# Performance work log

Measured on AMD Instinct MI355X. Metric: run time of the kernel, lower is better.

The kernel has to match this reference:

```python
import jax, jax.numpy as jnp
import numpy as np

H = 12          # n_heads
TYPE = 0        # center node type (query path)
EDGES = (0, 4, 5)  # useful_edge for type==0
NEG = -1e10
LN_EPS = 1e-5


def _type_emb(x, W, b, t):
    # Linear(E -> 2E), view [N,2,E], scatter-mask select type t (uniform type -> index)
    h = x @ W.T + b
    N = x.shape[0]
    E = W.shape[0] // 2
    return h.reshape(N, 2, E)[:, t, :]


def _layernorm(x, g, b):
    mu = jnp.mean(x, axis=-1, keepdims=True)
    var = jnp.mean((x - mu) ** 2, axis=-1, keepdims=True)
    return g * (x - mu) / jnp.sqrt(var + LN_EPS) + b


def setup_inputs() -> dict:
    B, L, E, R = 64, 64, 768, 8
    dk = E // H
    key = jax.random.key(0)
    ks = jax.random.split(key, 16)
    s = 0.02
    inp = {
        'center_ids': jax.random.randint(ks[0], (B, L), 0, 5000),
        'centers': jax.random.normal(ks[1], (B * L, E), jnp.float32),
        'all_embs': jax.random.normal(ks[2], (2 * B * L, E), jnp.float32),
        'pre_mask': (jax.random.uniform(ks[3], (B, L, L)) < 0.3).astype(jnp.float32),
        'back_mask': (jax.random.uniform(ks[4], (B, L, L)) < 0.3).astype(jnp.float32),
        'click_mask': (jax.random.uniform(ks[5], (B, L, L)) < 0.3).astype(jnp.float32),
        'blank': jnp.zeros((B, L, L), jnp.float32),
        'Wq': jax.random.normal(ks[6], (2 * E, E), jnp.float32) * s,
        'bq': jnp.zeros((2 * E,), jnp.float32),
        'Wk': jax.random.normal(ks[7], (2 * E, E), jnp.float32) * s,
        'bk': jnp.zeros((2 * E,), jnp.float32),
        'Wv': jax.random.normal(ks[8], (2 * E, E), jnp.float32) * s,
        'bv': jnp.zeros((2 * E,), jnp.float32),
        'Wa': jax.random.normal(ks[9], (2 * E, E), jnp.float32) * s,
        'ba': jnp.zeros((2 * E,), jnp.float32),
        'relation_pri': jnp.ones((R, H), jnp.float32),
        'relation_att': jax.random.normal(ks[10], (R, H, dk, dk), jnp.float32) / np.sqrt(dk),
        'relation_msg': jax.random.normal(ks[11], (R, H, dk, dk), jnp.float32) / np.sqrt(dk),
        'skip': jnp.ones((3,), jnp.float32),
        'ln_gamma': jnp.ones((E,), jnp.float32),
        'ln_beta': jnp.zeros((E,), jnp.float32),
    }
    return inp


def reference(center_ids, centers, all_embs, pre_mask, back_mask, click_mask, blank,
              Wq, bq, Wk, bk, Wv, bv, Wa, ba,
              relation_pri, relation_att, relation_msg, skip, ln_gamma, ln_beta):
    B, L = center_ids.shape
    E = centers.shape[-1]
    dk = E // H
    BL = B * L
    sqrt_dk = np.sqrt(dk).astype(np.float32)

    # type-masked QKV projections (q: all type 0; k,v: first BL type 0, second BL type 1)
    q = _type_emb(centers, Wq, bq, TYPE)                       # [BL, E]
    hk = (all_embs @ Wk.T + bk).reshape(2 * BL, 2, E)
    k = jnp.concatenate([hk[:BL, 0], hk[BL:, 1]], axis=0)      # [2BL, E]
    hv = (all_embs @ Wv.T + bv).reshape(2 * BL, 2, E)
    v = jnp.concatenate([hv[:BL, 0], hv[BL:, 1]], axis=0)      # [2BL, E]

    q4 = q.reshape(B, L, H, dk).transpose(2, 0, 1, 3)                          # [H,B,L,dk]
    k4 = k.reshape(2, B, L, H, dk).transpose(3, 1, 0, 2, 4).reshape(H, B, 2 * L, dk)
    v4 = v.reshape(2, B, L, H, dk).transpose(3, 1, 0, 2, 4).reshape(H, B, 2 * L, dk)

    eidx = jnp.array(EDGES)
    ra = relation_att[eidx]   # [3,H,dk,dk]
    rm = relation_msg[eidx]   # [3,H,dk,dk]
    pri = relation_pri[eidx]  # [3,H]

    kproj = jnp.einsum('hbtd,ehdf->ehbtf', k4, ra)                                  # [3,H,B,2L,dk]
    att = jnp.einsum('hbld,ehbtd->ehblt', q4, kproj) * pri[:, :, None, None, None] / sqrt_dk
    msg = jnp.einsum('hbtd,ehdf->ehbtf', v4, rm)                                    # [3,H,B,2L,dk]

    # flatten (kv_pos, edge) in the torch cat/view order: index = t*3 + e
    A = att.transpose(1, 2, 3, 4, 0).reshape(H, B, L, 2 * L * 3)
    msgf = msg.transpose(1, 2, 3, 0, 4).reshape(H, B, 2 * L * 3, dk)

    # per-edge masks for type==0: edge0 -> [blank|click], edge1 -> [back|blank], edge2 -> [pre|blank]
    m0 = jnp.concatenate([blank, click_mask], axis=-1)
    m1 = jnp.concatenate([back_mask, blank], axis=-1)
    m2 = jnp.concatenate([pre_mask, blank], axis=-1)
    mask = jnp.stack([m0, m1, m2], axis=-1).reshape(B, L, 2 * L * 3) > 0            # [B,L,TE]

    # share masks among identical center ids (equality is transitive => one matmul = closure)
    same = center_ids[:, :, None] == center_ids[:, None, :]                         # [B,L,L]
    repeat = jnp.triu(same, 1).sum(1) > 0                                           # [B,L]
    add = jnp.einsum('bil,blj->bij', same.astype(jnp.float32), mask.astype(jnp.float32)) > 0
    mask = (mask | add) & (~repeat[:, :, None])

    scores = jnp.where(mask[None], A, NEG)
    p = jax.nn.softmax(scores, axis=-1) * mask[None].astype(A.dtype)
    neigh = jnp.einsum('hblt,hbtd->hbld', p, msgf).transpose(1, 2, 0, 3).reshape(BL, E)
    neigh = jax.nn.gelu(neigh, approximate=False)

    retype = _type_emb(neigh, Wa, ba, TYPE)
    alpha = jax.nn.sigmoid(skip[TYPE])
    res = retype * alpha + centers * (1.0 - alpha)
    out = _layernorm(res, ln_gamma, ln_beta)
    return out.reshape(B, L, E)
```

## Files before the change

### kernel.cpp

```cpp
#include <hip/hip_runtime.h>
#include <cmath>

#define NEGV -1e10f

typedef __bf16 bf16_t;
typedef bf16_t bf16x8 __attribute__((ext_vector_type(8)));
typedef bf16_t bf16x4 __attribute__((ext_vector_type(4)));
typedef float f32x4 __attribute__((ext_vector_type(4)));

typedef const __attribute__((address_space(1))) void* gas1p;
typedef __attribute__((address_space(3))) void* las3p;

__global__ __launch_bounds__(256)
void f2b6_kernel(const float* __restrict__ s0, bf16_t* __restrict__ d0,
                 const float* __restrict__ s1, bf16_t* __restrict__ d1,
                 const float* __restrict__ s2, bf16_t* __restrict__ d2,
                 const float* __restrict__ s3, bf16_t* __restrict__ d3,
                 const float* __restrict__ s4, bf16_t* __restrict__ d4,
                 const float* __restrict__ s5, bf16_t* __restrict__ d5) {
  const int N0=786432, N1=1572864, N2=147456, N3=294912, N4=294912, N5=147456;
  const int T = N0+N1+N2+N3+N4+N5;
  int i = blockIdx.x * 256 + threadIdx.x;
  const int stride = gridDim.x * 256;
  for (; i < T; i += stride) {
    const float* s; bf16_t* d; int j = i;
    if (j < N0) { s = s0; d = d0; }
    else { j -= N0; if (j < N1) { s = s1; d = d1; }
    else { j -= N1; if (j < N2) { s = s2; d = d2; }
    else { j -= N2; if (j < N3) { s = s3; d = d3; }
    else { j -= N3; if (j < N4) { s = s4; d = d4; }
    else { j -= N4; s = s5; d = d5; } } } } }
    float4 v = *(const float4*)(s + (size_t)j * 4);
    bf16x4 o = { (bf16_t)v.x, (bf16_t)v.y, (bf16_t)v.z, (bf16_t)v.w };
    *(bf16x4*)(d + (size_t)j * 4) = o;
  }
}

__global__ __launch_bounds__(256)
void fold_rm(const float* __restrict__ rmsg, bf16_t* __restrict__ rmT) {
  const int eh = blockIdx.x;
  const int e = eh / 12, h = eh - e*12;
  const int re = (e==0) ? 0 : (e==1 ? 4 : 5);
  const int tid = threadIdx.x;
  for (int i = 0; i < 16; ++i) {
    int idx = i*256 + tid;
    int d = idx >> 6, f = idx & 63;
    rmT[((size_t)(e*12 + h)*64 + d)*64 + f] =
        (bf16_t)rmsg[((size_t)(re*12 + h)*64 + f)*64 + d];
  }
}

template<int NCOLS, int WSTRIDE, int BSTRIDE, int MHALF>
__global__ __launch_bounds__(256)
void proj_mfmaB(const bf16_t* __restrict__ X, const bf16_t* __restrict__ W,
                const float* __restrict__ bias, bf16_t* __restrict__ Y) {
  __shared__ bf16_t As[128 * 32];
  __shared__ bf16_t Bs[128 * 32];
  const int bn = blockIdx.x, bm = blockIdx.y;
  const int s = (MHALF && bm >= MHALF) ? 1 : 0;
  const int row0 = bm * 128, col0 = bn * 128;
  const int tid = threadIdx.x, wave = tid >> 6, lane = tid & 63;
  const int wr = wave >> 1, wc = wave & 1;
  f32x4 acc[4][4] = {};
  const int arow = wr * 64 + (lane & 15);
  const int bcol = wc * 64 + (lane & 15);
  const int koff = (lane >> 4) * 8;
  const bf16_t* Wb = W + (size_t)s * WSTRIDE;
  for (int k0 = 0; k0 < 768; k0 += 32) {
    __syncthreads();
    #pragma unroll
    for (int i = 0; i < 2; ++i) {
      int c = i * 256 + tid; int r = c >> 2; int c8 = (c & 3) * 8;
      __builtin_amdgcn_global_load_lds((gas1p)(X  + (size_t)(row0 + r) * 768 + k0 + c8),
                                       (las3p)(As + c * 8), 16, 0, 0);
      __builtin_amdgcn_global_load_lds((gas1p)(Wb + (size_t)(col0 + r) * 768 + k0 + c8),
                                       (las3p)(Bs + c * 8), 16, 0, 0);
    }
    __syncthreads();
    bf16x8 af[4], bfr[4];
    #pragma unroll
    for (int m = 0; m < 4; ++m) af[m]  = *(const bf16x8*)(As + (arow + m * 16) * 32 + koff);
    #pragma unroll
    for (int n = 0; n < 4; ++n) bfr[n] = *(const bf16x8*)(Bs + (bcol + n * 16) * 32 + koff);
    #pragma unroll
    for (int m = 0; m < 4; ++m)
      #pragma unroll
      for (int n = 0; n < 4; ++n)
        acc[m][n] = __builtin_amdgcn_mfma_f32_16x16x32_bf16(af[m], bfr[n], acc[m][n], 0, 0, 0);
  }
  const int ocol0 = col0 + wc * 64 + (lane & 15);
  const int orow0 = row0 + wr * 64 + (lane >> 4) * 4;
  #pragma unroll
  for (int n = 0; n < 4; ++n) {
    const int col = ocol0 + n * 16;
    const float bvl = bias[s * BSTRIDE + col];
    #pragma unroll
    for (int m = 0; m < 4; ++m)
      #pragma unroll
      for (int r = 0; r < 4; ++r)
        Y[(size_t)(orow0 + m * 16 + r) * NCOLS + col] = (bf16_t)(acc[m][n][r] + bvl);
  }
}

__global__ __launch_bounds__(256)
void proj_mfmaF(const bf16_t* __restrict__ X, const bf16_t* __restrict__ W,
                const float* __restrict__ bias, float* __restrict__ Y) {
  __shared__ bf16_t As[128 * 32];
  __shared__ bf16_t Bs[128 * 32];
  const int bn = blockIdx.x, bm = blockIdx.y;
  const int row0 = bm * 128, col0 = bn * 128;
  const int tid = threadIdx.x, wave = tid >> 6, lane = tid & 63;
  const int wr = wave >> 1, wc = wave & 1;
  f32x4 acc[4][4] = {};
  const int arow = wr * 64 + (lane & 15);
  const int bcol = wc * 64 + (lane & 15);
  const int koff = (lane >> 4) * 8;
  for (int k0 = 0; k0 < 768; k0 += 32) {
    __syncthreads();
    #pragma unroll
    for (int i = 0; i < 2; ++i) {
      int c = i * 256 + tid; int r = c >> 2; int c8 = (c & 3) * 8;
      __builtin_amdgcn_global_load_lds((gas1p)(X + (size_t)(row0 + r) * 768 + k0 + c8),
                                       (las3p)(As + c * 8), 16, 0, 0);
      __builtin_amdgcn_global_load_lds((gas1p)(W + (size_t)(col0 + r) * 768 + k0 + c8),
                                       (las3p)(Bs + c * 8), 16, 0, 0);
    }
    __syncthreads();
    bf16x8 af[4], bfr[4];
    #pragma unroll
    for (int m = 0; m < 4; ++m) af[m]  = *(const bf16x8*)(As + (arow + m * 16) * 32 + koff);
    #pragma unroll
    for (int n = 0; n < 4; ++n) bfr[n] = *(const bf16x8*)(Bs + (bcol + n * 16) * 32 + koff);
    #pragma unroll
    for (int m = 0; m < 4; ++m)
      #pragma unroll
      for (int n = 0; n < 4; ++n)
        acc[m][n] = __builtin_amdgcn_mfma_f32_16x16x32_bf16(af[m], bfr[n], acc[m][n], 0, 0, 0);
  }
  const int ocol0 = col0 + wc * 64 + (lane & 15);
  const int orow0 = row0 + wr * 64 + (lane >> 4) * 4;
  #pragma unroll
  for (int n = 0; n < 4; ++n) {
    const int col = ocol0 + n * 16;
    const float bvl = bias[col];
    #pragma unroll
    for (int m = 0; m < 4; ++m)
      #pragma unroll
      for (int r = 0; r < 4; ++r)
        Y[(size_t)(orow0 + m * 16 + r) * 768 + col] = acc[m][n][r] + bvl;
  }
}

template<int WSTRIDE, int BSTRIDE>
__global__ __launch_bounds__(256)
void projT(const bf16_t* __restrict__ X, const bf16_t* __restrict__ W,
           const float* __restrict__ bias, bf16_t* __restrict__ YT) {
  __shared__ bf16_t As[128 * 32];
  __shared__ bf16_t Bs[128 * 32];
  __shared__ char tl[128 * 256];
  const int bn = blockIdx.x, bm = blockIdx.y;
  const int s = (bm >= 32) ? 1 : 0;
  const int row0 = bm * 128, col0 = bn * 128;
  const int tid = threadIdx.x, wave = tid >> 6, lane = tid & 63;
  const int wr = wave >> 1, wc = wave & 1;
  f32x4 acc[4][4] = {};
  const int arow = wr * 64 + (lane & 15);
  const int bcol = wc * 64 + (lane & 15);
  const int koff = (lane >> 4) * 8;
  const bf16_t* Wb = W + (size_t)s * WSTRIDE;
  for (int k0 = 0; k0 < 768; k0 += 32) {
    __syncthreads();
    #pragma unroll
    for (int i = 0; i < 2; ++i) {
      int c = i * 256 + tid; int r = c >> 2; int c8 = (c & 3) * 8;
      __builtin_amdgcn_global_load_lds((gas1p)(X  + (size_t)(row0 + r) * 768 + k0 + c8),
                                       (las3p)(As + c * 8), 16, 0, 0);
      __builtin_amdgcn_global_load_lds((gas1p)(Wb + (size_t)(col0 + r) * 768 + k0 + c8),
                                       (las3p)(Bs + c * 8), 16, 0, 0);
    }
    __syncthreads();
    bf16x8 af[4], bfr[4];
    #pragma unroll
    for (int m = 0; m < 4; ++m) af[m]  = *(const bf16x8*)(As + (arow + m * 16) * 32 + koff);
    #pragma unroll
    for (int n = 0; n < 4; ++n) bfr[n] = *(const bf16x8*)(Bs + (bcol + n * 16) * 32 + koff);
    #pragma unroll
    for (int m = 0; m < 4; ++m)
      #pragma unroll
      for (int n = 0; n < 4; ++n)
        acc[m][n] = __builtin_amdgcn_mfma_f32_16x16x32_bf16(af[m], bfr[n], acc[m][n], 0, 0, 0);
  }
  __syncthreads();
  #pragma unroll
  for (int n = 0; n < 4; ++n) {
    const int cl = wc * 64 + n * 16 + (lane & 15);
    const float bvl = bias[s * BSTRIDE + col0 + cl];
    #pragma unroll
    for (int m = 0; m < 4; ++m)
      #pragma unroll
      for (int r = 0; r < 4; ++r) {
        const int rl = wr * 64 + m * 16 + (lane >> 4) * 4 + r;
        *(bf16_t*)(tl + ((cl * 256 + rl * 2) ^ ((cl & 7) << 4))) = (bf16_t)(acc[m][n][r] + bvl);
      }
  }
  __syncthreads();
  for (int i = 0; i < 8; ++i) {
    int idx = i * 256 + tid; int c = idx >> 4; int t0 = (idx & 15) * 8;
    bf16x8 v = *(const bf16x8*)(tl + ((c * 256 + t0 * 2) ^ ((c & 7) << 4)));
    *(bf16x8*)(YT + (size_t)(col0 + c) * 8192 + row0 + t0) = v;
  }
}

__global__ __launch_bounds__(256)
void qtrans_kernel(const bf16_t* __restrict__ qraw, const float* __restrict__ ratt,
                   const float* __restrict__ pri, bf16_t* __restrict__ qeb) {
  const int eh = blockIdx.x;
  const int e = eh / 12, h = eh - e*12;
  const int re = (e==0) ? 0 : (e==1 ? 4 : 5);
  const int row0 = blockIdx.y * 128;
  const float scale = pri[re*12 + h] * 0.125f;
  __shared__ char qls[128 * 128];
  __shared__ char rals[64 * 128];
  const int tid = threadIdx.x, wave = tid >> 6, lane = tid & 63;
  const int colb = lane & 15;
  for (int i = 0; i < 4; ++i) {
    int idx = i*256 + tid;
    int l = idx >> 3, f0 = (idx & 7) * 8;
    bf16x8 v = *(const bf16x8*)(qraw + (size_t)(row0 + l)*768 + h*64 + f0);
    *(bf16x8*)(qls + ((l*128 + f0*2) ^ ((l & 7) << 4))) = v;
  }
  for (int i = 0; i < 4; ++i) {
    int idx = i*256 + tid;
    int d = idx >> 4, f0 = (idx & 15) * 4;
    float4 v = *(const float4*)(ratt + ((size_t)(re*12 + h)*64 + d)*64 + f0);
    bf16x4 o = { (bf16_t)v.x, (bf16_t)v.y, (bf16_t)v.z, (bf16_t)v.w };
    *(bf16x4*)(rals + ((d*128 + f0*2) ^ ((d & 7) << 4))) = o;
  }
  __syncthreads();
  f32x4 acc[2][4] = {};
  #pragma unroll
  for (int ks = 0; ks < 2; ++ks) {
    const int kb2 = (ks*32 + (lane >> 4)*8) * 2;
    bf16x8 bfr[4];
    #pragma unroll
    for (int n = 0; n < 4; ++n) {
      int d = n*16 + colb;
      bfr[n] = *(const bf16x8*)(rals + ((d*128 + kb2) ^ ((d & 7) << 4)));
    }
    #pragma unroll
    for (int m = 0; m < 2; ++m) {
      int l = wave*32 + m*16 + colb;
      bf16x8 a = *(const bf16x8*)(qls + ((l*128 + kb2) ^ ((l & 7) << 4)));
      #pragma unroll
      for (int n = 0; n < 4; ++n)
        acc[m][n] = __builtin_amdgcn_mfma_f32_16x16x32_bf16(a, bfr[n], acc[m][n], 0, 0, 0);
    }
  }
  #pragma unroll
  for (int m = 0; m < 2; ++m)
    #pragma unroll
    for (int n = 0; n < 4; ++n)
      #pragma unroll
      for (int r = 0; r < 4; ++r) {
        int l = wave*32 + m*16 + (lane >> 4)*4 + r;
        int d = n*16 + colb;
        qeb[(size_t)(row0 + l)*2304 + (e*12 + h)*64 + d] = (bf16_t)(scale * acc[m][n][r]);
      }
}

__global__ __launch_bounds__(256)
void mask_kernel(const int* __restrict__ ids, const float* __restrict__ pre,
                 const float* __restrict__ back, const float* __restrict__ click,
                 unsigned long long* __restrict__ msk64) {
  const int b = blockIdx.x, tid = threadIdx.x;
  __shared__ float pm[64][68], bmm[64][68], cm[64][68];
  __shared__ unsigned long long sbits[64];
  __shared__ unsigned long long colbits[384];
  __shared__ int sid[64];
  __shared__ unsigned char srep[64];
  for (int r = 0; r < 4; ++r) {
    int idx = r*256 + tid; int row = idx >> 4; int c4 = (idx & 15) * 4;
    *(float4*)&pm[row][c4]  = *(const float4*)(pre   + (size_t)b*4096 + row*64 + c4);
    *(float4*)&bmm[row][c4] = *(const float4*)(back  + (size_t)b*4096 + row*64 + c4);
    *(float4*)&cm[row][c4]  = *(const float4*)(click + (size_t)b*4096 + row*64 + c4);
  }
  if (tid < 64) sid[tid] = ids[b*64 + tid];
  __syncthreads();
  if (tid < 64) {
    int myid = sid[tid];
    unsigned long long bits = 0ull; int rep = 0;
    for (int l = 0; l < 64; ++l) {
      bool eq = (sid[l] == myid);
      bits |= ((unsigned long long)eq) << l;
      rep |= (eq && (l < tid)) ? 1 : 0;
    }
    sbits[tid] = bits; srep[tid] = (unsigned char)rep;
  }
  for (int j = tid; j < 384; j += 256) {
    int e = j >> 7, t = j & 127;
    unsigned long long cb = 0ull;
    if (e == 0) {
      if (t >= 64) { int tt = t - 64; for (int l = 0; l < 64; ++l) cb |= ((unsigned long long)(cm[l][tt] > 0.0f)) << l; }
    } else if (e == 1) {
      if (t < 64) { for (int l = 0; l < 64; ++l) cb |= ((unsigned long long)(bmm[l][t] > 0.0f)) << l; }
    } else {
      if (t < 64) { for (int l = 0; l < 64; ++l) cb |= ((unsigned long long)(pm[l][t] > 0.0f)) << l; }
    }
    colbits[j] = cb;
  }
  __syncthreads();
  for (int idx = tid; idx < 384; idx += 256) {
    int l = idx / 6, w = idx - l*6;
    unsigned long long r = 0ull;
    if (!srep[l]) {
      unsigned long long sb = sbits[l];
      const int base = w*64;
      for (int jj = 0; jj < 64; ++jj)
        r |= (unsigned long long)((sb & colbits[base + jj]) != 0ull) << jj;
    }
    msk64[((size_t)(b*64) + l)*6 + w] = r;
  }
}

__global__ __launch_bounds__(256, 2)
void attn_fused(const bf16_t* __restrict__ qeb, const bf16_t* __restrict__ kb,
                const bf16_t* __restrict__ vT, const bf16_t* __restrict__ rmT,
                const unsigned long long* __restrict__ msk64,
                bf16_t* __restrict__ neigh) {
  const int h = blockIdx.x, b = blockIdx.y;
  __shared__ char kls[128 * 128];
  __shared__ char vls[64 * 256];
  __shared__ char rmls[3][64 * 128];
  __shared__ char pls[64 * 256];
  __shared__ char us[64 * 128];
  const int tid = threadIdx.x, wave = tid >> 6, lane = tid & 63;
  const int band = wave * 16;
  const int colb = lane & 15;
  for (int i = 0; i < 4; ++i) {
    int idx = i*256 + tid;
    int t = idx >> 3, c8 = (idx & 7) * 8;
    int srow = (t >> 6)*4096 + b*64 + (t & 63);
    bf16x8 v = *(const bf16x8*)(kb + (size_t)srow*768 + h*64 + c8);
    *(bf16x8*)(kls + ((t*128 + c8*2) ^ ((t & 7) << 4))) = v;
  }
  for (int i = 0; i < 4; ++i) {
    int idx = i*256 + tid;
    int f = idx >> 4, t0 = (idx & 15) * 8;
    bf16x8 v = *(const bf16x8*)(vT + (size_t)(h*64 + f)*8192 + (t0 >> 6)*4096 + b*64 + (t0 & 63));
    *(bf16x8*)(vls + ((f*256 + t0*2) ^ ((f & 7) << 4))) = v;
  }
  for (int i = 0; i < 6; ++i) {
    int idx = i*256 + tid;
    int e = idx >> 9, rem = idx & 511, d = rem >> 3, f0 = (rem & 7) * 8;
    bf16x8 v = *(const bf16x8*)(rmT + (size_t)((e*12 + h)*64 + d)*64 + f0);
    *(bf16x8*)(rmls[e] + ((d*128 + f0*2) ^ ((d & 7) << 4))) = v;
  }
  bf16x8 af[3][2];
  #pragma unroll
  for (int e = 0; e < 3; ++e)
    #pragma unroll
    for (int ks = 0; ks < 2; ++ks)
      af[e][ks] = *(const bf16x8*)(qeb + (size_t)(b*64 + band + colb)*2304
                                   + (e*12 + h)*64 + ks*32 + (lane >> 4)*8);
  __syncthreads();
  f32x4 acc[3][8] = {};
  #pragma unroll
  for (int ks = 0; ks < 2; ++ks) {
    bf16x8 bfr[8];
    #pragma unroll
    for (int n = 0; n < 8; ++n) {
      int t = n*16 + colb;
      bfr[n] = *(const bf16x8*)(kls + ((t*128 + (ks*32 + (lane >> 4)*8)*2) ^ ((t & 7) << 4)));
    }
    #pragma unroll
    for (int e = 0; e < 3; ++e)
      #pragma unroll
      for (int n = 0; n < 8; ++n)
        acc[e][n] = __builtin_amdgcn_mfma_f32_16x16x32_bf16(af[e][ks], bfr[n], acc[e][n], 0, 0, 0);
  }
  float mx[4], inv[4];
  #pragma unroll
  for (int r = 0; r < 4; ++r) {
    const int l = band + (lane >> 4)*4 + r;
    const unsigned long long* mr = msk64 + (size_t)(b*64 + l)*6;
    #pragma unroll
    for (int e = 0; e < 3; ++e) {
      unsigned long long w0 = mr[e*2], w1 = mr[e*2 + 1];
      #pragma unroll
      for (int n = 0; n < 8; ++n) {
        unsigned long long w = (n < 4) ? w0 : w1;
        int bitpos = (n*16 + colb) & 63;
        if (!((w >> bitpos) & 1ull)) acc[e][n][r] = NEGV;
      }
    }
  }
  #pragma unroll
  for (int r = 0; r < 4; ++r) {
    float m = NEGV;
    #pragma unroll
    for (int e = 0; e < 3; ++e)
      #pragma unroll
      for (int n = 0; n < 8; ++n) m = fmaxf(m, acc[e][n][r]);
    #pragma unroll
    for (int off = 1; off < 16; off <<= 1) m = fmaxf(m, __shfl_xor(m, off, 64));
    mx[r] = m;
  }
  #pragma unroll
  for (int r = 0; r < 4; ++r) {
    float s = 0.0f;
    #pragma unroll
    for (int e = 0; e < 3; ++e)
      #pragma unroll
      for (int n = 0; n < 8; ++n) {
        float v = __expf(acc[e][n][r] - mx[r]);
        acc[e][n][r] = v; s += v;
      }
    #pragma unroll
    for (int off = 1; off < 16; off <<= 1) s += __shfl_xor(s, off, 64);
    inv[r] = (mx[r] < -5e9f) ? 0.0f : 1.0f / s;
  }
  f32x4 accN[4] = {};
  #pragma unroll
  for (int e = 0; e < 3; ++e) {
    #pragma unroll
    for (int n = 0; n < 8; ++n)
      #pragma unroll
      for (int r = 0; r < 4; ++r) {
        int l = band + (lane >> 4)*4 + r;
        int t = n*16 + colb;
        *(bf16_t*)(pls + ((l*256 + t*2) ^ ((l & 7) << 4))) = (bf16_t)(acc[e][n][r] * inv[r]);
      }
    __syncthreads();
    f32x4 accU[4] = {};
    #pragma unroll
    for (int ks = 0; ks < 4; ++ks) {
      const int kb2 = (ks*32 + (lane >> 4)*8) * 2;
      const int la = band + colb;
      bf16x8 a = *(const bf16x8*)(pls + ((la*256 + kb2) ^ ((la & 7) << 4)));
      #pragma unroll
      for (int n = 0; n < 4; ++n) {
        int f = n*16 + colb;
        bf16x8 bv = *(const bf16x8*)(vls + ((f*256 + kb2) ^ ((f & 7) << 4)));
        accU[n] = __builtin_amdgcn_mfma_f32_16x16x32_bf16(a, bv, accU[n], 0, 0, 0);
      }
    }
    #pragma unroll
    for (int n = 0; n < 4; ++n)
      #pragma unroll
      for (int r = 0; r < 4; ++r) {
        int l = band + (lane >> 4)*4 + r;
        int f = n*16 + colb;
        *(bf16_t*)(us + ((l*128 + f*2) ^ ((l & 7) << 4))) = (bf16_t)accU[n][r];
      }
    __syncthreads();
    #pragma unroll
    for (int ks = 0; ks < 2; ++ks) {
      const int kb2 = (ks*32 + (lane >> 4)*8) * 2;
      const int la = band + colb;
      bf16x8 a2 = *(const bf16x8*)(us + ((la*128 + kb2) ^ ((la & 7) << 4)));
      #pragma unroll
      for (int n = 0; n < 4; ++n) {
        int d = n*16 + colb;
        bf16x8 brm = *(const bf16x8*)(rmls[e] + ((d*128 + kb2) ^ ((d & 7) << 4)));
        accN[n] = __builtin_amdgcn_mfma_f32_16x16x32_bf16(a2, brm, accN[n], 0, 0, 0);
      }
    }
  }
  #pragma unroll
  for (int n = 0; n < 4; ++n)
    #pragma unroll
    for (int r = 0; r < 4; ++r) {
      int l = band + (lane >> 4)*4 + r;
      int d = n*16 + colb;
      float x = accN[n][r];
      float g = 0.5f * x * (1.0f + erff(x * 0.70710678118654752f));
      neigh[(size_t)(b*64 + l)*768 + h*64 + d] = (bf16_t)g;
    }
}

__global__ __launch_bounds__(256)
void ln_kernel(const float* __restrict__ rt, const float* __restrict__ centers,
               const float* __restrict__ skip, const float* __restrict__ gamma,
               const float* __restrict__ beta, float* __restrict__ out) {
  const int row  = blockIdx.x*4 + (threadIdx.x >> 6);
  const int lane = threadIdx.x & 63;
  const float alpha = 1.0f / (1.0f + expf(-skip[0]));
  const float* rp = rt + (size_t)row*768;
  const float* cp = centers + (size_t)row*768;
  float r[12];
  float sum = 0.0f;
  #pragma unroll
  for (int c = 0; c < 12; ++c) {
    int j = lane + 64*c;
    float x = alpha*rp[j] + (1.0f - alpha)*cp[j];
    r[c] = x; sum += x;
  }
  #pragma unroll
  for (int off = 1; off < 64; off <<= 1) sum += __shfl_xor(sum, off, 64);
  float mean = sum * (1.0f/768.0f);
  float vsum = 0.0f;
  #pragma unroll
  for (int c = 0; c < 12; ++c) { float d = r[c] - mean; vsum += d*d; }
  #pragma unroll
  for (int off = 1; off < 64; off <<= 1) vsum += __shfl_xor(vsum, off, 64);
  float inv = 1.0f / sqrtf(vsum * (1.0f/768.0f) + 1e-5f);
  #pragma unroll
  for (int c = 0; c < 12; ++c) {
    int j = lane + 64*c;
    out[(size_t)row*768 + j] = gamma[j]*(r[c] - mean)*inv + beta[j];
  }
}

extern "C" void kernel_launch(void* const* d_in, const int* in_sizes, int n_in,
                              void* d_out, int out_size, void* d_ws, size_t ws_size,
                              hipStream_t stream) {
  const int*   ids     = (const int*)  d_in[0];
  const float* centers = (const float*)d_in[1];
  const float* allemb  = (const float*)d_in[2];
  const float* pre     = (const float*)d_in[3];
  const float* back    = (const float*)d_in[4];
  const float* click   = (const float*)d_in[5];
  const float* Wq = (const float*)d_in[7];
  const float* bq = (const float*)d_in[8];
  const float* Wk = (const float*)d_in[9];
  const float* bk = (const float*)d_in[10];
  const float* Wv = (const float*)d_in[11];
  const float* bv = (const float*)d_in[12];
  const float* Wa = (const float*)d_in[13];
  const float* ba = (const float*)d_in[14];
  const float* pri  = (const float*)d_in[15];
  const float* ratt = (const float*)d_in[16];
  const float* rmsg = (const float*)d_in[17];
  const float* skip = (const float*)d_in[18];
  const float* gam  = (const float*)d_in[19];
  const float* bet  = (const float*)d_in[20];
  float* out = (float*)d_out;

  char* wp = (char*)d_ws;
  bf16_t* cen_bf = (bf16_t*)wp;  wp += 6291456;
  bf16_t* all_bf = (bf16_t*)wp;  wp += 12582912;
  bf16_t* Wq_bf  = (bf16_t*)wp;  wp += 1179648;
  bf16_t* Wk_bf  = (bf16_t*)wp;  wp += 2359296;
  bf16_t* Wv_bf  = (bf16_t*)wp;  wp += 2359296;
  bf16_t* Wa_bf  = (bf16_t*)wp;  wp += 1179648;
  bf16_t* rmT    = (bf16_t*)wp;  wp += 294912;
  bf16_t* qraw   = (bf16_t*)wp;  wp += 6291456;
  bf16_t* qeb    = (bf16_t*)wp;  wp += 18874368;
  bf16_t* kb     = (bf16_t*)wp;  wp += 12582912;
  bf16_t* vTb    = (bf16_t*)wp;  wp += 12582912;
  unsigned long long* msk64 = (unsigned long long*)wp; wp += 196608;
  bf16_t* neighb = (bf16_t*)wp;  wp += 6291456;
  float*  rt     = (float*)wp;   wp += 12582912;

  f2b6_kernel<<<dim3(2048), 256, 0, stream>>>(centers, cen_bf, allemb, all_bf,
                                              Wq, Wq_bf, Wk, Wk_bf, Wv, Wv_bf, Wa, Wa_bf);
  fold_rm<<<dim3(36), 256, 0, stream>>>(rmsg, rmT);

  proj_mfmaB<768, 0, 0, 0>         <<<dim3(6, 32), 256, 0, stream>>>(cen_bf, Wq_bf, bq, qraw);
  qtrans_kernel                     <<<dim3(36, 32), 256, 0, stream>>>(qraw, ratt, pri, qeb);
  proj_mfmaB<768, 768*768, 768, 32><<<dim3(6, 64), 256, 0, stream>>>(all_bf, Wk_bf, bk, kb);
  projT<768*768, 768>              <<<dim3(6, 64), 256, 0, stream>>>(all_bf, Wv_bf, bv, vTb);

  mask_kernel<<<dim3(64), 256, 0, stream>>>(ids, pre, back, click, msk64);
  attn_fused<<<dim3(12, 64), 256, 0, stream>>>(qeb, kb, vTb, rmT, msk64, neighb);

  proj_mfmaF<<<dim3(6, 32), 256, 0, stream>>>(neighb, Wa_bf, ba, rt);
  ln_kernel<<<dim3(1024), 256, 0, stream>>>(rt, centers, skip, gam, bet, out);
}
```

Before: 271.0 us.

## Fuse prep kernels, merge K/V projections, and fold query relation transform into attention

Merges the mask build, relation-matrix folding and fp32-to-bf16 conversions into one prep launch. K and V projections now share a single kernel that loads each A tile once for both weight matrices. The per-relation query transform moves inside the attention kernel, which removes the qeb intermediate write and read and two launches. The costs are a larger LDS footprint in attention, which is reused through aliased regions, and extra register pressure from prefetching all operands into registers.

```diff
diff --git a/kernel.cpp b/kernel.cpp
--- a/kernel.cpp
+++ b/kernel.cpp
@@ -11,17 +11,91 @@
 typedef const __attribute__((address_space(1))) void* gas1p;
 typedef __attribute__((address_space(3))) void* las3p;
 
+#define MFMA __builtin_amdgcn_mfma_f32_16x16x32_bf16
+
 __global__ __launch_bounds__(256)
-void f2b6_kernel(const float* __restrict__ s0, bf16_t* __restrict__ d0,
+void prep_kernel(const int* __restrict__ ids, const float* __restrict__ pre,
+                 const float* __restrict__ back, const float* __restrict__ click,
+                 unsigned long long* __restrict__ msk64,
+                 const float* __restrict__ rmsg, const float* __restrict__ ratt,
+                 const float* __restrict__ pri, bf16_t* __restrict__ rmT, bf16_t* __restrict__ raB,
+                 const float* __restrict__ s0, bf16_t* __restrict__ d0,
                  const float* __restrict__ s1, bf16_t* __restrict__ d1,
                  const float* __restrict__ s2, bf16_t* __restrict__ d2,
                  const float* __restrict__ s3, bf16_t* __restrict__ d3,
                  const float* __restrict__ s4, bf16_t* __restrict__ d4,
                  const float* __restrict__ s5, bf16_t* __restrict__ d5) {
+  const int bid = blockIdx.x, tid = threadIdx.x;
+  __shared__ float pm[64][68], bmm[64][68], cm[64][68];
+  __shared__ unsigned long long sbits[64];
+  __shared__ unsigned long long colbits[384];
+  __shared__ int sid[64];
+  __shared__ unsigned char srep[64];
+  if (bid < 64) {
+    const int b = bid;
+    for (int r = 0; r < 4; ++r) {
+      int idx = r*256 + tid; int row = idx >> 4; int c4 = (idx & 15) * 4;
+      *(float4*)&pm[row][c4]  = *(const float4*)(pre   + (size_t)b*4096 + row*64 + c4);
+      *(float4*)&bmm[row][c4] = *(const float4*)(back  + (size_t)b*4096 + row*64 + c4);
+      *(float4*)&cm[row][c4]  = *(const float4*)(click + (size_t)b*4096 + row*64 + c4);
+    }
+    if (tid < 64) sid[tid] = ids[b*64 + tid];
+    __syncthreads();
+    if (tid < 64) {
+      int myid = sid[tid];
+      unsigned long long bits = 0ull; int rep = 0;
+      for (int l = 0; l < 64; ++l) {
+        bool eq = (sid[l] == myid);
+        bits |= ((unsigned long long)eq) << l;
+        rep |= (eq && (l < tid)) ? 1 : 0;
+      }
+      sbits[tid] = bits; srep[tid] = (unsigned char)rep;
+    }
+    for (int j = tid; j < 384; j += 256) {
+      int e = j >> 7, t = j & 127;
+      unsigned long long cb = 0ull;
+      if (e == 0) {
+        if (t >= 64) { int tt = t - 64; for (int l = 0; l < 64; ++l) cb |= ((unsigned long long)(cm[l][tt] > 0.0f)) << l; }
+      } else if (e == 1) {
+        if (t < 64) { for (int l = 0; l < 64; ++l) cb |= ((unsigned long long)(bmm[l][t] > 0.0f)) << l; }
+      } else {
+        if (t < 64) { for (int l = 0; l < 64; ++l) cb |= ((unsigned long long)(pm[l][t] > 0.0f)) << l; }
+      }
+      colbits[j] = cb;
+    }
+    __syncthreads();
+    for (int idx = tid; idx < 384; idx += 256) {
+      int l = idx / 6, w = idx - l*6;
+      unsigned long long r = 0ull;
+      if (!srep[l]) {
+        unsigned long long sb = sbits[l];
+        const int base = w*64;
+        for (int jj = 0; jj < 64; ++jj)
+          r |= (unsigned long long)((sb & colbits[base + jj]) != 0ull) << jj;
+      }
+      msk64[((size_t)(b*64) + l)*6 + w] = r;
+    }
+    return;
+  }
+  if (bid < 100) {
+    const int eh = bid - 64;
+    const int e = eh / 12, h = eh - e*12;
+    const int re = (e==0) ? 0 : (e==1 ? 4 : 5);
+    const float scale = pri[re*12 + h] * 0.125f;
+    for (int i = 0; i < 16; ++i) {
+      int idx = i*256 + tid;
+      int d = idx >> 6, f = idx & 63;
+      rmT[((size_t)(e*12 + h)*64 + d)*64 + f] =
+          (bf16_t)rmsg[((size_t)(re*12 + h)*64 + f)*64 + d];
+      raB[((size_t)(e*12 + h)*64 + d)*64 + f] =
+          (bf16_t)(ratt[((size_t)(re*12 + h)*64 + d)*64 + f] * scale);
+    }
+    return;
+  }
   const int N0=786432, N1=1572864, N2=147456, N3=294912, N4=294912, N5=147456;
   const int T = N0+N1+N2+N3+N4+N5;
-  int i = blockIdx.x * 256 + threadIdx.x;
-  const int stride = gridDim.x * 256;
+  int i = (bid - 100) * 256 + tid;
+  const int stride = (gridDim.x - 100) * 256;
   for (; i < T; i += stride) {
     const float* s; bf16_t* d; int j = i;
     if (j < N0) { s = s0; d = d0; }
@@ -37,27 +111,11 @@
 }
 
 __global__ __launch_bounds__(256)
-void fold_rm(const float* __restrict__ rmsg, bf16_t* __restrict__ rmT) {
-  const int eh = blockIdx.x;
-  const int e = eh / 12, h = eh - e*12;
-  const int re = (e==0) ? 0 : (e==1 ? 4 : 5);
-  const int tid = threadIdx.x;
-  for (int i = 0; i < 16; ++i) {
-    int idx = i*256 + tid;
-    int d = idx >> 6, f = idx & 63;
-    rmT[((size_t)(e*12 + h)*64 + d)*64 + f] =
-        (bf16_t)rmsg[((size_t)(re*12 + h)*64 + f)*64 + d];
-  }
-}
-
-template<int NCOLS, int WSTRIDE, int BSTRIDE, int MHALF>
-__global__ __launch_bounds__(256)
 void proj_mfmaB(const bf16_t* __restrict__ X, const bf16_t* __restrict__ W,
                 const float* __restrict__ bias, bf16_t* __restrict__ Y) {
   __shared__ bf16_t As[128 * 32];
   __shared__ bf16_t Bs[128 * 32];
   const int bn = blockIdx.x, bm = blockIdx.y;
-  const int s = (MHALF && bm >= MHALF) ? 1 : 0;
   const int row0 = bm * 128, col0 = bn * 128;
   const int tid = threadIdx.x, wave = tid >> 6, lane = tid & 63;
   const int wr = wave >> 1, wc = wave & 1;
@@ -65,15 +123,14 @@
   const int arow = wr * 64 + (lane & 15);
   const int bcol = wc * 64 + (lane & 15);
   const int koff = (lane >> 4) * 8;
-  const bf16_t* Wb = W + (size_t)s * WSTRIDE;
   for (int k0 = 0; k0 < 768; k0 += 32) {
     __syncthreads();
     #pragma unroll
     for (int i = 0; i < 2; ++i) {
       int c = i * 256 + tid; int r = c >> 2; int c8 = (c & 3) * 8;
-      __builtin_amdgcn_global_load_lds((gas1p)(X  + (size_t)(row0 + r) * 768 + k0 + c8),
+      __builtin_amdgcn_global_load_lds((gas1p)(X + (size_t)(row0 + r) * 768 + k0 + c8),
                                        (las3p)(As + c * 8), 16, 0, 0);
-      __builtin_amdgcn_global_load_lds((gas1p)(Wb + (size_t)(col0 + r) * 768 + k0 + c8),
+      __builtin_amdgcn_global_load_lds((gas1p)(W + (size_t)(col0 + r) * 768 + k0 + c8),
                                        (las3p)(Bs + c * 8), 16, 0, 0);
     }
     __syncthreads();
@@ -86,19 +143,19 @@
     for (int m = 0; m < 4; ++m)
       #pragma unroll
       for (int n = 0; n < 4; ++n)
-        acc[m][n] = __builtin_amdgcn_mfma_f32_16x16x32_bf16(af[m], bfr[n], acc[m][n], 0, 0, 0);
+        acc[m][n] = MFMA(af[m], bfr[n], acc[m][n], 0, 0, 0);
   }
   const int ocol0 = col0 + wc * 64 + (lane & 15);
   const int orow0 = row0 + wr * 64 + (lane >> 4) * 4;
   #pragma unroll
   for (int n = 0; n < 4; ++n) {
     const int col = ocol0 + n * 16;
-    const float bvl = bias[s * BSTRIDE + col];
+    const float bvl = bias[col];
     #pragma unroll
     for (int m = 0; m < 4; ++m)
       #pragma unroll
       for (int r = 0; r < 4; ++r)
-        Y[(size_t)(orow0 + m * 16 + r) * NCOLS + col] = (bf16_t)(acc[m][n][r] + bvl);
+        Y[(size_t)(orow0 + m * 16 + r) * 768 + col] = (bf16_t)(acc[m][n][r] + bvl);
   }
 }
 
@@ -135,7 +192,7 @@
     for (int m = 0; m < 4; ++m)
       #pragma unroll
       for (int n = 0; n < 4; ++n)
-        acc[m][n] = __builtin_amdgcn_mfma_f32_16x16x32_bf16(af[m], bfr[n], acc[m][n], 0, 0, 0);
+        acc[m][n] = MFMA(af[m], bfr[n], acc[m][n], 0, 0, 0);
   }
   const int ocol0 = col0 + wc * 64 + (lane & 15);
   const int orow0 = row0 + wr * 64 + (lane >> 4) * 4;
@@ -151,217 +208,172 @@
   }
 }
 
-template<int WSTRIDE, int BSTRIDE>
 __global__ __launch_bounds__(256)
-void projT(const bf16_t* __restrict__ X, const bf16_t* __restrict__ W,
-           const float* __restrict__ bias, bf16_t* __restrict__ YT) {
+void kv_proj(const bf16_t* __restrict__ X, const bf16_t* __restrict__ Wk,
+             const bf16_t* __restrict__ Wv, const float* __restrict__ bk,
+             const float* __restrict__ bv, bf16_t* __restrict__ K, bf16_t* __restrict__ VT) {
   __shared__ bf16_t As[128 * 32];
-  __shared__ bf16_t Bs[128 * 32];
+  __shared__ bf16_t Bks[128 * 32];
+  __shared__ bf16_t Bvs[128 * 32];
   __shared__ char tl[128 * 256];
   const int bn = blockIdx.x, bm = blockIdx.y;
   const int s = (bm >= 32) ? 1 : 0;
   const int row0 = bm * 128, col0 = bn * 128;
   const int tid = threadIdx.x, wave = tid >> 6, lane = tid & 63;
   const int wr = wave >> 1, wc = wave & 1;
-  f32x4 acc[4][4] = {};
+  f32x4 acck[4][4] = {};
+  f32x4 accv[4][4] = {};
   const int arow = wr * 64 + (lane & 15);
   const int bcol = wc * 64 + (lane & 15);
   const int koff = (lane >> 4) * 8;
-  const bf16_t* Wb = W + (size_t)s * WSTRIDE;
+  const bf16_t* Wkb = Wk + (size_t)s * 768 * 768;
+  const bf16_t* Wvb = Wv + (size_t)s * 768 * 768;
   for (int k0 = 0; k0 < 768; k0 += 32) {
     __syncthreads();
     #pragma unroll
     for (int i = 0; i < 2; ++i) {
       int c = i * 256 + tid; int r = c >> 2; int c8 = (c & 3) * 8;
-      __builtin_amdgcn_global_load_lds((gas1p)(X  + (size_t)(row0 + r) * 768 + k0 + c8),
-                                       (las3p)(As + c * 8), 16, 0, 0);
-      __builtin_amdgcn_global_load_lds((gas1p)(Wb + (size_t)(col0 + r) * 768 + k0 + c8),
-                                       (las3p)(Bs + c * 8), 16, 0, 0);
-    }
-    __syncthreads();
-    bf16x8 af[4], bfr[4];
-    #pragma unroll
-    for (int m = 0; m < 4; ++m) af[m]  = *(const bf16x8*)(As + (arow + m * 16) * 32 + koff);
-    #pragma unroll
-    for (int n = 0; n < 4; ++n) bfr[n] = *(const bf16x8*)(Bs + (bcol + n * 16) * 32 + koff);
-    #pragma unroll
-    for (int m = 0; m < 4; ++m)
-      #pragma unroll
-      for (int n = 0; n < 4; ++n)
-        acc[m][n] = __builtin_amdgcn_mfma_f32_16x16x32_bf16(af[m], bfr[n], acc[m][n], 0, 0, 0);
-  }
-  __syncthreads();
+      __builtin_amdgcn_global_load_lds((gas1p)(X   + (size_t)(row0 + r) * 768 + k0 + c8),
+                                       (las3p)(As  + c * 8), 16, 0, 0);
+      __builtin_amdgcn_global_load_lds((gas1p)(Wkb + (size_t)(col0 + r) * 768 + k0 + c8),
+                                       (las3p)(Bks + c * 8), 16, 0, 0);
+      __builtin_amdgcn_global_load_lds((gas1p)(Wvb + (size_t)(col0 + r) * 768 + k0 + c8),
+                                       (las3p)(Bvs + c * 8), 16, 0, 0);
+    }
+    __syncthreads();
+    bf16x8 af[4], bk_[4], bv_[4];
+    #pragma unroll
+    for (int m = 0; m < 4; ++m) af[m]  = *(const bf16x8*)(As  + (arow + m * 16) * 32 + koff);
+    #pragma unroll
+    for (int n = 0; n < 4; ++n) { bk_[n] = *(const bf16x8*)(Bks + (bcol + n * 16) * 32 + koff);
+                                  bv_[n] = *(const bf16x8*)(Bvs + (bcol + n * 16) * 32 + koff); }
+    #pragma unroll
+    for (int m = 0; m < 4; ++m)
+      #pragma unroll
+      for (int n = 0; n < 4; ++n) {
+        acck[m][n] = MFMA(af[m], bk_[n], acck[m][n], 0, 0, 0);
+        accv[m][n] = MFMA(af[m], bv_[n], accv[m][n], 0, 0, 0);
+      }
+  }
+  const int ocol0 = col0 + wc * 64 + (lane & 15);
+  const int orow0 = row0 + wr * 64 + (lane >> 4) * 4;
+  #pragma unroll
+  for (int n = 0; n < 4; ++n) {
+    const int col = ocol0 + n * 16;
+    const float bvl = bk[s * 768 + col];
+    #pragma unroll
+    for (int m = 0; m < 4; ++m)
+      #pragma unroll
+      for (int r = 0; r < 4; ++r)
+        K[(size_t)(orow0 + m * 16 + r) * 768 + col] = (bf16_t)(acck[m][n][r] + bvl);
+  }
   #pragma unroll
   for (int n = 0; n < 4; ++n) {
     const int cl = wc * 64 + n * 16 + (lane & 15);
-    const float bvl = bias[s * BSTRIDE + col0 + cl];
+    const float bvl = bv[s * 768 + col0 + cl];
     #pragma unroll
     for (int m = 0; m < 4; ++m)
       #pragma unroll
       for (int r = 0; r < 4; ++r) {
         const int rl = wr * 64 + m * 16 + (lane >> 4) * 4 + r;
-        *(bf16_t*)(tl + ((cl * 256 + rl * 2) ^ ((cl & 7) << 4))) = (bf16_t)(acc[m][n][r] + bvl);
+        *(bf16_t*)(tl + ((cl * 256 + rl * 2) ^ ((cl & 7) << 4))) = (bf16_t)(accv[m][n][r] + bvl);
       }
   }
   __syncthreads();
   for (int i = 0; i < 8; ++i) {
     int idx = i * 256 + tid; int c = idx >> 4; int t0 = (idx & 15) * 8;
     bf16x8 v = *(const bf16x8*)(tl + ((c * 256 + t0 * 2) ^ ((c & 7) << 4)));
-    *(bf16x8*)(YT + (size_t)(col0 + c) * 8192 + row0 + t0) = v;
-  }
-}
-
-__global__ __launch_bounds__(256)
-void qtrans_kernel(const bf16_t* __restrict__ qraw, const float* __restrict__ ratt,
-                   const float* __restrict__ pri, bf16_t* __restrict__ qeb) {
-  const int eh = blockIdx.x;
-  const int e = eh / 12, h = eh - e*12;
-  const int re = (e==0) ? 0 : (e==1 ? 4 : 5);
-  const int row0 = blockIdx.y * 128;
-  const float scale = pri[re*12 + h] * 0.125f;
-  __shared__ char qls[128 * 128];
-  __shared__ char rals[64 * 128];
+    *(bf16x8*)(VT + (size_t)(col0 + c) * 8192 + row0 + t0) = v;
+  }
+}
+
+__global__ __launch_bounds__(256, 2)
+void attn_fused2(const bf16_t* __restrict__ qraw, const bf16_t* __restrict__ kb,
+                 const bf16_t* __restrict__ vT, const bf16_t* __restrict__ rmT,
+                 const bf16_t* __restrict__ raB,
+                 const unsigned long long* __restrict__ msk64,
+                 bf16_t* __restrict__ neigh) {
+  const int h = blockIdx.x, b = blockIdx.y;
+  __shared__ char lds[81920];
+  char* const QLS  = lds;
+  char* const RALS = lds + 8192;
+  char* const QELS = lds + 32768;
+  char* const VLS  = lds;
+  char* const PLS  = lds + 16384;
+  char* const KLS  = lds + 32768;
+  char* const RMLS = lds + 49152;
+  char* const USS  = lds + 73728;
   const int tid = threadIdx.x, wave = tid >> 6, lane = tid & 63;
-  const int colb = lane & 15;
-  for (int i = 0; i < 4; ++i) {
-    int idx = i*256 + tid;
-    int l = idx >> 3, f0 = (idx & 7) * 8;
-    bf16x8 v = *(const bf16x8*)(qraw + (size_t)(row0 + l)*768 + h*64 + f0);
-    *(bf16x8*)(qls + ((l*128 + f0*2) ^ ((l & 7) << 4))) = v;
-  }
-  for (int i = 0; i < 4; ++i) {
-    int idx = i*256 + tid;
-    int d = idx >> 4, f0 = (idx & 15) * 4;
-    float4 v = *(const float4*)(ratt + ((size_t)(re*12 + h)*64 + d)*64 + f0);
-    bf16x4 o = { (bf16_t)v.x, (bf16_t)v.y, (bf16_t)v.z, (bf16_t)v.w };
-    *(bf16x4*)(rals + ((d*128 + f0*2) ^ ((d & 7) << 4))) = o;
-  }
+  const int band = wave * 16, colb = lane & 15;
+
+  bf16x8 qreg[2], rareg[6], kreg[4], vreg[4], rmreg[6];
+  #pragma unroll
+  for (int i = 0; i < 2; ++i) { int idx = i*256 + tid; int l = idx >> 3, f0 = (idx & 7) * 8;
+    qreg[i] = *(const bf16x8*)(qraw + (size_t)(b*64 + l)*768 + h*64 + f0); }
+  #pragma unroll
+  for (int i = 0; i < 6; ++i) { int idx = i*256 + tid; int e = idx >> 9, rem = idx & 511, d = rem >> 3, f0 = (rem & 7) * 8;
+    rareg[i] = *(const bf16x8*)(raB + (size_t)((e*12 + h)*64 + d)*64 + f0); }
+  #pragma unroll
+  for (int i = 0; i < 4; ++i) { int idx = i*256 + tid; int t = idx >> 3, c8 = (idx & 7) * 8;
+    int srow = (t >> 6)*4096 + b*64 + (t & 63);
+    kreg[i] = *(const bf16x8*)(kb + (size_t)srow*768 + h*64 + c8); }
+  #pragma unroll
+  for (int i = 0; i < 4; ++i) { int idx = i*256 + tid; int f = idx >> 4, t0 = (idx & 15) * 8;
+    vreg[i] = *(const bf16x8*)(vT + (size_t)(h*64 + f)*8192 + (t0 >> 6)*4096 + b*64 + (t0 & 63)); }
+  #pragma unroll
+  for (int i = 0; i < 6; ++i) { int idx = i*256 + tid; int e = idx >> 9, rem = idx & 511, d = rem >> 3, f0 = (rem & 7) * 8;
+    rmreg[i] = *(const bf16x8*)(rmT + (size_t)((e*12 + h)*64 + d)*64 + f0); }
+
+  #pragma unroll
+  for (int i = 0; i < 2; ++i) { int idx = i*256 + tid; int l = idx >> 3, f0 = (idx & 7) * 8;
+    *(bf16x8*)(QLS + ((l*128 + f0*2) ^ ((l & 7) << 4))) = qreg[i]; }
+  #pragma unroll
+  for (int i = 0; i < 6; ++i) { int idx = i*256 + tid; int e = idx >> 9, rem = idx & 511, d = rem >> 3, f0 = (rem & 7) * 8;
+    *(bf16x8*)(RALS + e*8192 + ((d*128 + f0*2) ^ ((d & 7) << 4))) = rareg[i]; }
   __syncthreads();
-  f32x4 acc[2][4] = {};
+  f32x4 accq[3][4] = {};
   #pragma unroll
   for (int ks = 0; ks < 2; ++ks) {
     const int kb2 = (ks*32 + (lane >> 4)*8) * 2;
-    bf16x8 bfr[4];
-    #pragma unroll
-    for (int n = 0; n < 4; ++n) {
-      int d = n*16 + colb;
-      bfr[n] = *(const bf16x8*)(rals + ((d*128 + kb2) ^ ((d & 7) << 4)));
-    }
-    #pragma unroll
-    for (int m = 0; m < 2; ++m) {
-      int l = wave*32 + m*16 + colb;
-      bf16x8 a = *(const bf16x8*)(qls + ((l*128 + kb2) ^ ((l & 7) << 4)));
-      #pragma unroll
-      for (int n = 0; n < 4; ++n)
-        acc[m][n] = __builtin_amdgcn_mfma_f32_16x16x32_bf16(a, bfr[n], acc[m][n], 0, 0, 0);
-    }
-  }
-  #pragma unroll
-  for (int m = 0; m < 2; ++m)
+    const int la = band + colb;
+    bf16x8 a = *(const bf16x8*)(QLS + ((la*128 + kb2) ^ ((la & 7) << 4)));
+    #pragma unroll
+    for (int e = 0; e < 3; ++e)
+      #pragma unroll
+      for (int n = 0; n < 4; ++n) {
+        int d = n*16 + colb;
+        bf16x8 bf = *(const bf16x8*)(RALS + e*8192 + ((d*128 + kb2) ^ ((d & 7) << 4)));
+        accq[e][n] = MFMA(a, bf, accq[e][n], 0, 0, 0);
+      }
+  }
+  #pragma unroll
+  for (int e = 0; e < 3; ++e)
     #pragma unroll
     for (int n = 0; n < 4; ++n)
       #pragma unroll
       for (int r = 0; r < 4; ++r) {
-        int l = wave*32 + m*16 + (lane >> 4)*4 + r;
-        int d = n*16 + colb;
-        qeb[(size_t)(row0 + l)*2304 + (e*12 + h)*64 + d] = (bf16_t)(scale * acc[m][n][r]);
-      }
-}
-
-__global__ __launch_bounds__(256)
-void mask_kernel(const int* __restrict__ ids, const float* __restrict__ pre,
-                 const float* __restrict__ back, const float* __restrict__ click,
-                 unsigned long long* __restrict__ msk64) {
-  const int b = blockIdx.x, tid = threadIdx.x;
-  __shared__ float pm[64][68], bmm[64][68], cm[64][68];
-  __shared__ unsigned long long sbits[64];
-  __shared__ unsigned long long colbits[384];
-  __shared__ int sid[64];
-  __shared__ unsigned char srep[64];
-  for (int r = 0; r < 4; ++r) {
-    int idx = r*256 + tid; int row = idx >> 4; int c4 = (idx & 15) * 4;
-    *(float4*)&pm[row][c4]  = *(const float4*)(pre   + (size_t)b*4096 + row*64 + c4);
-    *(float4*)&bmm[row][c4] = *(const float4*)(back  + (size_t)b*4096 + row*64 + c4);
-    *(float4*)&cm[row][c4]  = *(const float4*)(click + (size_t)b*4096 + row*64 + c4);
-  }
-  if (tid < 64) sid[tid] = ids[b*64 + tid];
+        int l = band + (lane >> 4)*4 + r, d = n*16 + colb;
+        *(bf16_t*)(QELS + e*8192 + ((l*128 + d*2) ^ ((l & 7) << 4))) = (bf16_t)accq[e][n][r];
+      }
   __syncthreads();
-  if (tid < 64) {
-    int myid = sid[tid];
-    unsigned long long bits = 0ull; int rep = 0;
-    for (int l = 0; l < 64; ++l) {
-      bool eq = (sid[l] == myid);
-      bits |= ((unsigned long long)eq) << l;
-      rep |= (eq && (l < tid)) ? 1 : 0;
-    }
-    sbits[tid] = bits; srep[tid] = (unsigned char)rep;
-  }
-  for (int j = tid; j < 384; j += 256) {
-    int e = j >> 7, t = j & 127;
-    unsigned long long cb = 0ull;
-    if (e == 0) {
-      if (t >= 64) { int tt = t - 64; for (int l = 0; l < 64; ++l) cb |= ((unsigned long long)(cm[l][tt] > 0.0f)) << l; }
-    } else if (e == 1) {
-      if (t < 64) { for (int l = 0; l < 64; ++l) cb |= ((unsigned long long)(bmm[l][t] > 0.0f)) << l; }
-    } else {
-      if (t < 64) { for (int l = 0; l < 64; ++l) cb |= ((unsigned long long)(pm[l][t] > 0.0f)) << l; }
-    }
-    colbits[j] = cb;
-  }
+  bf16x8 af[3][2];
+  #pragma unroll
+  for (int e = 0; e < 3; ++e)
+    #pragma unroll
+    for (int ks = 0; ks < 2; ++ks) {
+      int la = band + colb, kd2 = (ks*32 + (lane >> 4)*8) * 2;
+      af[e][ks] = *(const bf16x8*)(QELS + e*8192 + ((la*128 + kd2) ^ ((la & 7) << 4)));
+    }
   __syncthreads();
-  for (int idx = tid; idx < 384; idx += 256) {
-    int l = idx / 6, w = idx - l*6;
-    unsigned long long r = 0ull;
-    if (!srep[l]) {
-      unsigned long long sb = sbits[l];
-      const int base = w*64;
-      for (int jj = 0; jj < 64; ++jj)
-        r |= (unsigned long long)((sb & colbits[base + jj]) != 0ull) << jj;
-    }
-    msk64[((size_t)(b*64) + l)*6 + w] = r;
-  }
-}
-
-__global__ __launch_bounds__(256, 2)
-void attn_fused(const bf16_t* __restrict__ qeb, const bf16_t* __restrict__ kb,
-                const bf16_t* __restrict__ vT, const bf16_t* __restrict__ rmT,
-                const unsigned long long* __restrict__ msk64,
-                bf16_t* __restrict__ neigh) {
-  const int h = blockIdx.x, b = blockIdx.y;
-  __shared__ char kls[128 * 128];
-  __shared__ char vls[64 * 256];
-  __shared__ char rmls[3][64 * 128];
-  __shared__ char pls[64 * 256];
-  __shared__ char us[64 * 128];
-  const int tid = threadIdx.x, wave = tid >> 6, lane = tid & 63;
-  const int band = wave * 16;
-  const int colb = lane & 15;
-  for (int i = 0; i < 4; ++i) {
-    int idx = i*256 + tid;
-    int t = idx >> 3, c8 = (idx & 7) * 8;
-    int srow = (t >> 6)*4096 + b*64 + (t & 63);
-    bf16x8 v = *(const bf16x8*)(kb + (size_t)srow*768 + h*64 + c8);
-    *(bf16x8*)(kls + ((t*128 + c8*2) ^ ((t & 7) << 4))) = v;
-  }
-  for (int i = 0; i < 4; ++i) {
-    int idx = i*256 + tid;
-    int f = idx >> 4, t0 = (idx & 15) * 8;
-    bf16x8 v = *(const bf16x8*)(vT + (size_t)(h*64 + f)*8192 + (t0 >> 6)*4096 + b*64 + (t0 & 63));
-    *(bf16x8*)(vls + ((f*256 + t0*2) ^ ((f & 7) << 4))) = v;
-  }
-  for (int i = 0; i < 6; ++i) {
-    int idx = i*256 + tid;
-    int e = idx >> 9, rem = idx & 511, d = rem >> 3, f0 = (rem & 7) * 8;
-    bf16x8 v = *(const bf16x8*)(rmT + (size_t)((e*12 + h)*64 + d)*64 + f0);
-    *(bf16x8*)(rmls[e] + ((d*128 + f0*2) ^ ((d & 7) << 4))) = v;
-  }
-  bf16x8 af[3][2];
-  #pragma unroll
-  for (int e = 0; e < 3; ++e)
-    #pragma unroll
-    for (int ks = 0; ks < 2; ++ks)
-      af[e][ks] = *(const bf16x8*)(qeb + (size_t)(b*64 + band + colb)*2304
-                                   + (e*12 + h)*64 + ks*32 + (lane >> 4)*8);
+  #pragma unroll
+  for (int i = 0; i < 4; ++i) { int idx = i*256 + tid; int t = idx >> 3, c8 = (idx & 7) * 8;
+    *(bf16x8*)(KLS + ((t*128 + c8*2) ^ ((t & 7) << 4))) = kreg[i]; }
+  #pragma unroll
+  for (int i = 0; i < 4; ++i) { int idx = i*256 + tid; int f = idx >> 4, t0 = (idx & 15) * 8;
+    *(bf16x8*)(VLS + ((f*256 + t0*2) ^ ((f & 7) << 4))) = vreg[i]; }
+  #pragma unroll
+  for (int i = 0; i < 6; ++i) { int idx = i*256 + tid; int e = idx >> 9, rem = idx & 511, d = rem >> 3, f0 = (rem & 7) * 8;
+    *(bf16x8*)(RMLS + e*8192 + ((d*128 + f0*2) ^ ((d & 7) << 4))) = rmreg[i]; }
   __syncthreads();
   f32x4 acc[3][8] = {};
   #pragma unroll
@@ -370,13 +382,13 @@
     #pragma unroll
     for (int n = 0; n < 8; ++n) {
       int t = n*16 + colb;
-      bfr[n] = *(const bf16x8*)(kls + ((t*128 + (ks*32 + (lane >> 4)*8)*2) ^ ((t & 7) << 4)));
+      bfr[n] = *(const bf16x8*)(KLS + ((t*128 + (ks*32 + (lane >> 4)*8)*2) ^ ((t & 7) << 4)));
     }
     #pragma unroll
     for (int e = 0; e < 3; ++e)
       #pragma unroll
       for (int n = 0; n < 8; ++n)
-        acc[e][n] = __builtin_amdgcn_mfma_f32_16x16x32_bf16(af[e][ks], bfr[n], acc[e][n], 0, 0, 0);
+        acc[e][n] = MFMA(af[e][ks], bfr[n], acc[e][n], 0, 0, 0);
   }
   float mx[4], inv[4];
   #pragma unroll
@@ -428,7 +440,7 @@
       for (int r = 0; r < 4; ++r) {
         int l = band + (lane >> 4)*4 + r;
         int t = n*16 + colb;
-        *(bf16_t*)(pls + ((l*256 + t*2) ^ ((l & 7) << 4))) = (bf16_t)(acc[e][n][r] * inv[r]);
+        *(bf16_t*)(PLS + ((l*256 + t*2) ^ ((l & 7) << 4))) = (bf16_t)(acc[e][n][r] * inv[r]);
       }
     __syncthreads();
     f32x4 accU[4] = {};
@@ -436,12 +448,12 @@
     for (int ks = 0; ks < 4; ++ks) {
       const int kb2 = (ks*32 + (lane >> 4)*8) * 2;
       const int la = band + colb;
-      bf16x8 a = *(const bf16x8*)(pls + ((la*256 + kb2) ^ ((la & 7) << 4)));
+      bf16x8 a = *(const bf16x8*)(PLS + ((la*256 + kb2) ^ ((la & 7) << 4)));
       #pragma unroll
       for (int n = 0; n < 4; ++n) {
         int f = n*16 + colb;
-        bf16x8 bv = *(const bf16x8*)(vls + ((f*256 + kb2) ^ ((f & 7) << 4)));
-        accU[n] = __builtin_amdgcn_mfma_f32_16x16x32_bf16(a, bv, accU[n], 0, 0, 0);
+        bf16x8 bv = *(const bf16x8*)(VLS + ((f*256 + kb2) ^ ((f & 7) << 4)));
+        accU[n] = MFMA(a, bv, accU[n], 0, 0, 0);
       }
     }
     #pragma unroll
@@ -450,19 +462,19 @@
       for (int r = 0; r < 4; ++r) {
         int l = band + (lane >> 4)*4 + r;
         int f = n*16 + colb;
-        *(bf16_t*)(us + ((l*128 + f*2) ^ ((l & 7) << 4))) = (bf16_t)accU[n][r];
+        *(bf16_t*)(USS + ((l*128 + f*2) ^ ((l & 7) << 4))) = (bf16_t)accU[n][r];
       }
     __syncthreads();
     #pragma unroll
     for (int ks = 0; ks < 2; ++ks) {
       const int kb2 = (ks*32 + (lane >> 4)*8) * 2;
       const int la = band + colb;
-      bf16x8 a2 = *(const bf16x8*)(us + ((la*128 + kb2) ^ ((la & 7) << 4)));
+      bf16x8 a2 = *(const bf16x8*)(USS + ((la*128 + kb2) ^ ((la & 7) << 4)));
       #pragma unroll
       for (int n = 0; n < 4; ++n) {
         int d = n*16 + colb;
-        bf16x8 brm = *(const bf16x8*)(rmls[e] + ((d*128 + kb2) ^ ((d & 7) << 4)));
-        accN[n] = __builtin_amdgcn_mfma_f32_16x16x32_bf16(a2, brm, accN[n], 0, 0, 0);
+        bf16x8 brm = *(const bf16x8*)(RMLS + e*8192 + ((d*128 + kb2) ^ ((d & 7) << 4)));
+        accN[n] = MFMA(a2, brm, accN[n], 0, 0, 0);
       }
     }
   }
@@ -544,25 +556,22 @@
   bf16_t* Wv_bf  = (bf16_t*)wp;  wp += 2359296;
   bf16_t* Wa_bf  = (bf16_t*)wp;  wp += 1179648;
   bf16_t* rmT    = (bf16_t*)wp;  wp += 294912;
+  bf16_t* raB    = (bf16_t*)wp;  wp += 294912;
   bf16_t* qraw   = (bf16_t*)wp;  wp += 6291456;
-  bf16_t* qeb    = (bf16_t*)wp;  wp += 18874368;
   bf16_t* kb     = (bf16_t*)wp;  wp += 12582912;
   bf16_t* vTb    = (bf16_t*)wp;  wp += 12582912;
   unsigned long long* msk64 = (unsigned long long*)wp; wp += 196608;
   bf16_t* neighb = (bf16_t*)wp;  wp += 6291456;
   float*  rt     = (float*)wp;   wp += 12582912;
 
-  f2b6_kernel<<<dim3(2048), 256, 0, stream>>>(centers, cen_bf, allemb, all_bf,
-                                              Wq, Wq_bf, Wk, Wk_bf, Wv, Wv_bf, Wa, Wa_bf);
-  fold_rm<<<dim3(36), 256, 0, stream>>>(rmsg, rmT);
-
-  proj_mfmaB<768, 0, 0, 0>         <<<dim3(6, 32), 256, 0, stream>>>(cen_bf, Wq_bf, bq, qraw);
-  qtrans_kernel                     <<<dim3(36, 32), 256, 0, stream>>>(qraw, ratt, pri, qeb);
-  proj_mfmaB<768, 768*768, 768, 32><<<dim3(6, 64), 256, 0, stream>>>(all_bf, Wk_bf, bk, kb);
-  projT<768*768, 768>              <<<dim3(6, 64), 256, 0, stream>>>(all_bf, Wv_bf, bv, vTb);
-
-  mask_kernel<<<dim3(64), 256, 0, stream>>>(ids, pre, back, click, msk64);
-  attn_fused<<<dim3(12, 64), 256, 0, stream>>>(qeb, kb, vTb, rmT, msk64, neighb);
+  prep_kernel<<<dim3(2048), 256, 0, stream>>>(
+      ids, pre, back, click, msk64, rmsg, ratt, pri, rmT, raB,
+      centers, cen_bf, allemb, all_bf, Wq, Wq_bf, Wk, Wk_bf, Wv, Wv_bf, Wa, Wa_bf);
+
+  proj_mfmaB<<<dim3(6, 32), 256, 0, stream>>>(cen_bf, Wq_bf, bq, qraw);
+  kv_proj   <<<dim3(6, 64), 256, 0, stream>>>(all_bf, Wk_bf, Wv_bf, bk, bv, kb, vTb);
+
+  attn_fused2<<<dim3(12, 64), 256, 0, stream>>>(qraw, kb, vTb, rmT, raB, msk64, neighb);
 
   proj_mfmaF<<<dim3(6, 32), 256, 0, stream>>>(neighb, Wa_bf, ba, rt);
   ln_kernel<<<dim3(1024), 256, 0, stream>>>(rt, centers, skip, gam, bet, out);
```

After: 266.8 us. About the same (-1.5%).
